# Kernel optimization log

Hardware: AMD Instinct MI355X
Metric: run time of the kernel (lower is better)

Reference implementation:

```python
import jax, jax.numpy as jnp
import numpy as np
from jax.scipy.special import logsumexp

NUM_TAGS = 64
BATCH = 512
SEQ = 1024


def setup_inputs() -> dict:
    key = jax.random.key(0)
    k1, k2, k3, k4, k5 = jax.random.split(key, 5)
    emissions = jax.random.normal(k1, (BATCH, SEQ, NUM_TAGS), dtype=jnp.float32)
    # parameters: uniform(-0.1, 0.1) as in reset_parameters
    start_transitions = jax.random.uniform(k2, (NUM_TAGS,), minval=-0.1, maxval=0.1, dtype=jnp.float32)
    end_transitions = jax.random.uniform(k3, (NUM_TAGS,), minval=-0.1, maxval=0.1, dtype=jnp.float32)
    transitions = jax.random.uniform(k4, (NUM_TAGS, NUM_TAGS), minval=-0.1, maxval=0.1, dtype=jnp.float32)
    tags = jax.random.randint(k5, (BATCH, SEQ), 0, NUM_TAGS, dtype=jnp.int64)
    mask = jnp.ones((BATCH, SEQ), dtype=bool)
    return {"emissions": emissions, "start_transitions": start_transitions,
            "end_transitions": end_transitions, "transitions": transitions,
            "tags": tags, "mask": mask}


def _crf_loss(emissions, start_transitions, end_transitions, transitions, tags, mask):
    # batch_first=True -> move to time-major (S, B, T)
    emissions = jnp.transpose(emissions, (1, 0, 2))
    tags = tags.T
    mask = mask.T
    S, B, T = emissions.shape
    maskf = mask.astype(emissions.dtype)

    # ---- joint (numerator) score, fully vectorized ----
    em_sc = jnp.take_along_axis(emissions, tags[:, :, None], axis=2)[:, :, 0]  # [S, B]
    trans_sc = transitions[tags[:-1], tags[1:]]                                # [S-1, B]
    score = start_transitions[tags[0]] + em_sc[0]
    score = score + ((trans_sc + em_sc[1:]) * maskf[1:]).sum(axis=0)
    seq_ends = mask.astype(jnp.int32).sum(axis=0) - 1                          # [B]
    last_tags = tags[seq_ends, jnp.arange(B)]
    score = score + end_transitions[last_tags]

    # ---- log partition (denominator) via scan over time ----
    def step(alphas, xs):
        em_i, m_i = xs  # em_i: [B, T], m_i: [B]
        inner = alphas[:, :, None] + transitions[None, :, :] + em_i[:, None, :]  # [B, T, T]
        new_alphas = logsumexp(inner, axis=1)
        return jnp.where(m_i[:, None], new_alphas, alphas), None

    alphas0 = start_transitions + emissions[0]  # [B, T]
    alphas, _ = jax.lax.scan(step, alphas0, (emissions[1:], mask[1:]))
    log_z = logsumexp(alphas + end_transitions, axis=1)  # [B]

    return (log_z - score).sum()  # reduction='sum'


def reference(emissions, start_transitions, end_transitions, transitions, tags, mask):
    return _crf_loss(emissions, start_transitions, end_transitions, transitions, tags, mask)
```

## Files before the change

### kernel.cpp

```cpp
#include <hip/hip_runtime.h>

#define NT 64
#define SEQ 1024
#define BATCH 512

typedef float v2f __attribute__((ext_vector_type(2)));
typedef float v4f __attribute__((ext_vector_type(4)));

__device__ __forceinline__ float rlf(float v, int lane) {
  return __int_as_float(__builtin_amdgcn_readlane(__float_as_int(v), lane));
}

__global__ __launch_bounds__(64) void crf_fwd(
    const float* __restrict__ em,
    const float* __restrict__ startT,
    const float* __restrict__ endT,
    const float* __restrict__ trans,
    const int*   __restrict__ tags,
    float* __restrict__ ws)
{
  const int b = blockIdx.x;
  const int j = threadIdx.x;

  __shared__ float sT[NT * NT];
  __shared__ float sB[NT];
  for (int i = j; i < NT * NT; i += NT) sT[i] = trans[i];
  __syncthreads();

  v2f et2[NT / 2];
  #pragma unroll
  for (int p = 0; p < NT / 2; ++p) {
    et2[p].x = __expf(sT[(2 * p + 0) * NT + j]) * 0.015625f;
    et2[p].y = __expf(sT[(2 * p + 1) * NT + j]) * 0.015625f;
  }

  const float* emb = em + (size_t)b * SEQ * NT;
  const int*   tgb = tags + (size_t)b * SEQ;

  const float alpha0 = startT[j] + emb[j];
  const float c0 = rlf(alpha0, 0);
  float beta = __expf(alpha0 - c0);
  sB[j] = beta;
  float Crn = 0.0f;

  int tagv = tgb[j];
  const int tag0 = __builtin_amdgcn_readlane(tagv, 0);
  const float sc0 = rlf(alpha0, tag0);

  float emsc = 0.0f;
  float trsc = 0.0f;
  int carry;
  {
    int ptag = __shfl_up(tagv, 1);
    trsc += (j == 0) ? 0.0f : sT[ptag * NT + tagv];
    carry = __builtin_amdgcn_readlane(tagv, 63);
  }

  float embuf[8];
  #pragma unroll
  for (int k = 1; k <= 8; ++k) embuf[k & 7] = emb[k * NT + j];

  auto step = [&](int s, int slot, int r, bool renorm) {
    const float em_cur = embuf[slot];
    int spre = s + 8;
    if (spre > SEQ - 1) spre = SEQ - 1;
    embuf[slot] = emb[spre * NT + j];

    const float m = __expf(em_cur - 0.5f);

    v2f a0 = {0.f, 0.f}, a1 = {0.f, 0.f}, a2 = {0.f, 0.f}, a3 = {0.f, 0.f};
    #pragma unroll
    for (int q = 0; q < 16; q += 2) {
      const v4f ev0 = *reinterpret_cast<const v4f*>(&sB[4 * q]);
      const v4f ev1 = *reinterpret_cast<const v4f*>(&sB[4 * q + 4]);
      v2f lo0 = {ev0.x, ev0.y}, hi0 = {ev0.z, ev0.w};
      v2f lo1 = {ev1.x, ev1.y}, hi1 = {ev1.z, ev1.w};
      a0 = __builtin_elementwise_fma(lo0, et2[2 * q + 0], a0);
      a1 = __builtin_elementwise_fma(hi0, et2[2 * q + 1], a1);
      a2 = __builtin_elementwise_fma(lo1, et2[2 * q + 2], a2);
      a3 = __builtin_elementwise_fma(hi1, et2[2 * q + 3], a3);
    }
    const v2f at = (a0 + a1) + (a2 + a3);
    float nb = (at.x + at.y) * m;

    if (renorm) {
      const float rv = rlf(nb, 0);
      const float rr = __builtin_amdgcn_rcpf(rv);
      nb *= rr;
      Crn += __logf(rv) - __logf(rr * rv);
    }
    beta = nb;
    sB[j] = nb;

    const int tg = __builtin_amdgcn_readlane(tagv, r);
    emsc += rlf(em_cur, tg);
  };

  #pragma unroll 8
  for (int r = 0; r < NT; ++r) {
    if (r > 0) step(r, r & 7, r, (r & 7) == 7);
  }

  for (int tb = 1; tb < SEQ / NT; ++tb) {
    tagv = tgb[tb * NT + j];
    int ptag = __shfl_up(tagv, 1);
    if (j == 0) ptag = carry;
    trsc += sT[ptag * NT + tagv];
    carry = __builtin_amdgcn_readlane(tagv, 63);

    const int base = tb * NT;
    #pragma unroll 8
    for (int r = 0; r < NT; ++r) {
      step(base + r, r & 7, r, (r & 7) == 7);
    }
  }

  const float endv = endT[j];
  const float x = beta * __expf(endv);
  float tot = 0.f;
  #pragma unroll
  for (int i = 0; i < NT; ++i) tot += rlf(x, i);
  const float Cbase = c0 + (float)(SEQ - 1) * (0.5f + 4.1588830833596715f);
  const float logz = Cbase + Crn + __logf(tot);

  float trtot = 0.f;
  #pragma unroll
  for (int i = 0; i < NT; ++i) trtot += rlf(trsc, i);

  const int tlast = carry;
  const float score = sc0 + emsc + trtot + rlf(endv, tlast);

  if (j == 0) ws[b] = logz - score;
}

__global__ __launch_bounds__(64) void reduce_loss(const float* __restrict__ ws,
                                                  float* __restrict__ out) {
  const int t = threadIdx.x;
  float v = 0.f;
  #pragma unroll
  for (int k = 0; k < BATCH / 64; ++k) v += ws[k * 64 + t];
  float tot = 0.f;
  #pragma unroll
  for (int i = 0; i < 64; ++i) tot += rlf(v, i);
  if (t == 0) out[0] = tot;
}

extern "C" void kernel_launch(void* const* d_in, const int* in_sizes, int n_in,
                              void* d_out, int out_size, void* d_ws, size_t ws_size,
                              hipStream_t stream) {
  const float* em    = (const float*)d_in[0];
  const float* st    = (const float*)d_in[1];
  const float* en    = (const float*)d_in[2];
  const float* tr    = (const float*)d_in[3];
  const int*   tags  = (const int*)d_in[4];

  float* ws  = (float*)d_ws;
  float* out = (float*)d_out;

  crf_fwd<<<BATCH, 64, 0, stream>>>(em, st, en, tr, tags, ws);
  reduce_loss<<<1, 64, 0, stream>>>(ws, out);
}
```

Baseline: 365.8 us.

## Use fp16 dot2 for CRF forward recurrence with per-step deferred renormalization

The per-step 64x64 matvec now keeps the exponentiated transition matrix and the shared beta vector in fp16 and accumulates with packed fdot2 instructions into fp32. This halves the LDS traffic and the FMA instruction count on the serial critical path. Renormalization now happens every step, but the reciprocal is applied one step later so it is off the dependency chain. The emission score gather moves out of the inner step into a per-block gather, and the lane reductions switch to xor-shuffle trees. The fp16 storage of beta and transitions reduces accuracy and risks overflow or underflow for larger inputs.

```diff
diff --git a/kernel.cpp b/kernel.cpp
--- a/kernel.cpp
+++ b/kernel.cpp
@@ -4,11 +4,23 @@
 #define SEQ 1024
 #define BATCH 512
 
-typedef float v2f __attribute__((ext_vector_type(2)));
-typedef float v4f __attribute__((ext_vector_type(4)));
+typedef _Float16 h2 __attribute__((ext_vector_type(2)));
+typedef _Float16 h8 __attribute__((ext_vector_type(8)));
 
 __device__ __forceinline__ float rlf(float v, int lane) {
   return __int_as_float(__builtin_amdgcn_readlane(__float_as_int(v), lane));
+}
+__device__ __forceinline__ float bsum(float v) {
+  #pragma unroll
+  for (int m = 32; m; m >>= 1) v += __shfl_xor(v, m);
+  return v;
+}
+__device__ __forceinline__ float dot2(h2 a, h2 b, float c) {
+#if __has_builtin(__builtin_amdgcn_fdot2)
+  return __builtin_amdgcn_fdot2(a, b, c, false);
+#else
+  return fmaf((float)a[0], (float)b[0], fmaf((float)a[1], (float)b[1], c));
+#endif
 }
 
 __global__ __launch_bounds__(64) void crf_fwd(
@@ -23,112 +35,103 @@
   const int j = threadIdx.x;
 
   __shared__ float sT[NT * NT];
-  __shared__ float sB[NT];
+  __shared__ alignas(16) _Float16 sH[NT];
   for (int i = j; i < NT * NT; i += NT) sT[i] = trans[i];
   __syncthreads();
 
-  v2f et2[NT / 2];
+  h2 eth[NT / 2];
   #pragma unroll
   for (int p = 0; p < NT / 2; ++p) {
-    et2[p].x = __expf(sT[(2 * p + 0) * NT + j]) * 0.015625f;
-    et2[p].y = __expf(sT[(2 * p + 1) * NT + j]) * 0.015625f;
+    eth[p][0] = (_Float16)(__expf(sT[(2 * p + 0) * NT + j]) * 0.015625f);
+    eth[p][1] = (_Float16)(__expf(sT[(2 * p + 1) * NT + j]) * 0.015625f);
   }
 
   const float* emb = em + (size_t)b * SEQ * NT;
   const int*   tgb = tags + (size_t)b * SEQ;
 
-  const float alpha0 = startT[j] + emb[j];
+  const float stv = startT[j];
+  const float alpha0 = stv + emb[j];
   const float c0 = rlf(alpha0, 0);
-  float beta = __expf(alpha0 - c0);
-  sB[j] = beta;
+  float nb = __expf(alpha0 - c0);
+  sH[j] = (_Float16)nb;
+
   float Crn = 0.0f;
+  float rr = 1.0f;
+  float lgrr = 0.0f;
 
   int tagv = tgb[j];
   const int tag0 = __builtin_amdgcn_readlane(tagv, 0);
-  const float sc0 = rlf(alpha0, tag0);
+  const float sc0 = rlf(stv, tag0);
 
-  float emsc = 0.0f;
-  float trsc = 0.0f;
-  int carry;
+  float scp = 0.0f;
   {
     int ptag = __shfl_up(tagv, 1);
-    trsc += (j == 0) ? 0.0f : sT[ptag * NT + tagv];
-    carry = __builtin_amdgcn_readlane(tagv, 63);
+    if (j > 0) scp += sT[ptag * NT + tagv];
+    scp += emb[j * NT + tagv];
   }
+  int carry = __builtin_amdgcn_readlane(tagv, 63);
 
   float embuf[8];
   #pragma unroll
   for (int k = 1; k <= 8; ++k) embuf[k & 7] = emb[k * NT + j];
 
-  auto step = [&](int s, int slot, int r, bool renorm) {
+  auto step = [&](int s, int slot) {
     const float em_cur = embuf[slot];
     int spre = s + 8;
     if (spre > SEQ - 1) spre = SEQ - 1;
     embuf[slot] = emb[spre * NT + j];
 
-    const float m = __expf(em_cur - 0.5f);
+    const float mm = __expf(em_cur - 0.5f) * rr;
+    Crn -= lgrr;
 
-    v2f a0 = {0.f, 0.f}, a1 = {0.f, 0.f}, a2 = {0.f, 0.f}, a3 = {0.f, 0.f};
+    float a[8];
     #pragma unroll
-    for (int q = 0; q < 16; q += 2) {
-      const v4f ev0 = *reinterpret_cast<const v4f*>(&sB[4 * q]);
-      const v4f ev1 = *reinterpret_cast<const v4f*>(&sB[4 * q + 4]);
-      v2f lo0 = {ev0.x, ev0.y}, hi0 = {ev0.z, ev0.w};
-      v2f lo1 = {ev1.x, ev1.y}, hi1 = {ev1.z, ev1.w};
-      a0 = __builtin_elementwise_fma(lo0, et2[2 * q + 0], a0);
-      a1 = __builtin_elementwise_fma(hi0, et2[2 * q + 1], a1);
-      a2 = __builtin_elementwise_fma(lo1, et2[2 * q + 2], a2);
-      a3 = __builtin_elementwise_fma(hi1, et2[2 * q + 3], a3);
+    for (int q = 0; q < 8; ++q) {
+      const h8 wv = *reinterpret_cast<const h8*>(&sH[8 * q]);
+      const h2 w0 = __builtin_shufflevector(wv, wv, 0, 1);
+      const h2 w1 = __builtin_shufflevector(wv, wv, 2, 3);
+      const h2 w2 = __builtin_shufflevector(wv, wv, 4, 5);
+      const h2 w3 = __builtin_shufflevector(wv, wv, 6, 7);
+      float acc = dot2(w0, eth[4 * q + 0], 0.0f);
+      acc = dot2(w1, eth[4 * q + 1], acc);
+      acc = dot2(w2, eth[4 * q + 2], acc);
+      acc = dot2(w3, eth[4 * q + 3], acc);
+      a[q] = acc;
     }
-    const v2f at = (a0 + a1) + (a2 + a3);
-    float nb = (at.x + at.y) * m;
+    const float s01 = (a[0] + a[1]) + (a[2] + a[3]);
+    const float s23 = (a[4] + a[5]) + (a[6] + a[7]);
+    nb = (s01 + s23) * mm;
+    sH[j] = (_Float16)nb;
 
-    if (renorm) {
-      const float rv = rlf(nb, 0);
-      const float rr = __builtin_amdgcn_rcpf(rv);
-      nb *= rr;
-      Crn += __logf(rv) - __logf(rr * rv);
-    }
-    beta = nb;
-    sB[j] = nb;
-
-    const int tg = __builtin_amdgcn_readlane(tagv, r);
-    emsc += rlf(em_cur, tg);
+    const float rv = rlf(nb, 0);
+    rr = __builtin_amdgcn_rcpf(rv);
+    lgrr = __logf(rr);
   };
 
   #pragma unroll 8
-  for (int r = 0; r < NT; ++r) {
-    if (r > 0) step(r, r & 7, r, (r & 7) == 7);
-  }
+  for (int r = 1; r < NT; ++r) step(r, r & 7);
 
   for (int tb = 1; tb < SEQ / NT; ++tb) {
     tagv = tgb[tb * NT + j];
     int ptag = __shfl_up(tagv, 1);
     if (j == 0) ptag = carry;
-    trsc += sT[ptag * NT + tagv];
+    scp += sT[ptag * NT + tagv];
+    const int base = tb * NT;
+    scp += emb[(base + j) * NT + tagv];
     carry = __builtin_amdgcn_readlane(tagv, 63);
 
-    const int base = tb * NT;
     #pragma unroll 8
-    for (int r = 0; r < NT; ++r) {
-      step(base + r, r & 7, r, (r & 7) == 7);
-    }
+    for (int r = 0; r < NT; ++r) step(base + r, r & 7);
   }
 
   const float endv = endT[j];
-  const float x = beta * __expf(endv);
-  float tot = 0.f;
-  #pragma unroll
-  for (int i = 0; i < NT; ++i) tot += rlf(x, i);
+  const float x = nb * __expf(endv);
+  const float tot = bsum(x);
   const float Cbase = c0 + (float)(SEQ - 1) * (0.5f + 4.1588830833596715f);
   const float logz = Cbase + Crn + __logf(tot);
 
-  float trtot = 0.f;
-  #pragma unroll
-  for (int i = 0; i < NT; ++i) trtot += rlf(trsc, i);
-
-  const int tlast = carry;
-  const float score = sc0 + emsc + trtot + rlf(endv, tlast);
+  const float sctot = bsum(scp);
+  const float score = sc0 + sctot + rlf(endv, carry);
 
   if (j == 0) ws[b] = logz - score;
 }
@@ -139,9 +142,7 @@
   float v = 0.f;
   #pragma unroll
   for (int k = 0; k < BATCH / 64; ++k) v += ws[k * 64 + t];
-  float tot = 0.f;
-  #pragma unroll
-  for (int i = 0; i < 64; ++i) tot += rlf(v, i);
+  const float tot = bsum(v);
   if (t == 0) out[0] = tot;
 }
 
```

Result: no change. 363.8 us (-0.5%).
